# Kernel optimization log

Hardware: AMD Instinct MI355X
Metric: run time of the kernel (lower is better)

## Reference

```python
import jax, jax.numpy as jnp
import numpy as np

EMBED_DIM = 1024
NUM_HEADS = 16
HEAD_DIM = EMBED_DIM // NUM_HEADS
LN_EPS = 1e-12
B, S = 2, 2048


def setup_inputs() -> dict:
    key = jax.random.key(0)
    ks = jax.random.split(key, 12)
    scale = 1.0 / np.sqrt(EMBED_DIM)
    d = EMBED_DIM
    return {
        "in_features": jax.random.normal(ks[0], (B, S, d), dtype=jnp.float32),
        "tgt_mask": jnp.ones((B, S), dtype=jnp.float32),
        "Wq": jax.random.normal(ks[1], (d, d), dtype=jnp.float32) * scale,
        "bq": jnp.zeros((d,), dtype=jnp.float32),
        "Wk": jax.random.normal(ks[2], (d, d), dtype=jnp.float32) * scale,
        "bk": jnp.zeros((d,), dtype=jnp.float32),
        "Wv": jax.random.normal(ks[3], (d, d), dtype=jnp.float32) * scale,
        "bv": jnp.zeros((d,), dtype=jnp.float32),
        "Wo": jax.random.normal(ks[4], (d, d), dtype=jnp.float32) * scale,
        "bo": jnp.zeros((d,), dtype=jnp.float32),
        "gamma": jnp.ones((d,), dtype=jnp.float32),
        "beta": jnp.zeros((d,), dtype=jnp.float32),
    }


def _split_heads(x):  # [B,S,D] -> [B,H,S,Dh]
    b, s, _ = x.shape
    return x.reshape(b, s, NUM_HEADS, HEAD_DIM).transpose(0, 2, 1, 3)


def reference(in_features, tgt_mask, Wq, bq, Wk, bk, Wv, bv, Wo, bo, gamma, beta):
    # Self-attention (tgt_features defaults to in_features). Dropout in eval mode (identity).
    q = _split_heads(in_features @ Wq.T + bq)
    k = _split_heads(in_features @ Wk.T + bk)
    v = _split_heads(in_features @ Wv.T + bv)
    # scores: [B,H,S,S]
    scores = jnp.einsum("bhqd,bhkd->bhqk", q, k) / jnp.sqrt(jnp.float32(HEAD_DIM))
    scores = scores + (1.0 - tgt_mask)[:, None, None, :] * (-100000.0)
    attn = jax.nn.softmax(scores, axis=-1)
    ctx = jnp.einsum("bhqk,bhkd->bhqd", attn, v)  # [B,H,S,Dh]
    ctx = ctx.transpose(0, 2, 1, 3).reshape(in_features.shape)  # merge heads
    out = ctx @ Wo.T + bo
    x = out + in_features
    mu = jnp.mean(x, axis=-1, keepdims=True)
    var = jnp.mean(jnp.square(x - mu), axis=-1, keepdims=True)
    return (x - mu) / jnp.sqrt(var + LN_EPS) * gamma + beta
```

## Files before the change

### kernel.cpp

```cpp
#include <hip/hip_runtime.h>
#include <hip/hip_bf16.h>

#define DM   1024
#define HEADS 16
#define DH    64
#define SEQ  2048
#define BATCH   2
#define LOG2E 1.44269504088896f

typedef __attribute__((ext_vector_type(8))) short short8;
typedef __attribute__((ext_vector_type(4))) short bf16x4;
typedef __attribute__((ext_vector_type(4))) float floatx4;
typedef __attribute__((ext_vector_type(16))) float floatx16;

__device__ __forceinline__ short f2b(float f) {
    union { float f; unsigned u; } v; v.f = f;
    unsigned r = v.u + 0x7FFFu + ((v.u >> 16) & 1u);
    return (short)(r >> 16);
}

#if __has_builtin(__builtin_amdgcn_exp2f)
__device__ __forceinline__ float fexp2(float x) { return __builtin_amdgcn_exp2f(x); }
#else
__device__ __forceinline__ float fexp2(float x) { return exp2f(x); }
#endif

__device__ __forceinline__ void async_copy16(const short* gsrc, short* ldst) {
    __builtin_amdgcn_global_load_lds(
        (const __attribute__((address_space(1))) void*)gsrc,
        (__attribute__((address_space(3))) void*)ldst,
        16, 0, 0);
}

__global__ __launch_bounds__(256) void cvt_all(const float* __restrict__ x,
        const float* __restrict__ wq, const float* __restrict__ wk,
        const float* __restrict__ wv, const float* __restrict__ wo,
        const float* __restrict__ mask,
        short* __restrict__ xb, short* __restrict__ wqkv, short* __restrict__ wob,
        float* __restrict__ maddg)
{
    const int b = blockIdx.x;
    if (b >= 8192) {
        const int bb = b - 8192;
        const float* mrow = mask + (size_t)bb * SEQ;
        float* mg = maddg + (size_t)bb * SEQ;
#pragma unroll
        for (int i = 0; i < 8; ++i) {
            const int idx = threadIdx.x * 8 + i;
            mg[idx] = (1.f - mrow[idx]) * (-100000.f * LOG2E);
        }
        return;
    }
    const float* src; short* dst; int idx;
    if (b < 4096)      { src = x;  dst = xb;                idx = b; }
    else if (b < 5120) { src = wq; dst = wqkv;              idx = b - 4096; }
    else if (b < 6144) { src = wk; dst = wqkv + (1 << 20);  idx = b - 5120; }
    else if (b < 7168) { src = wv; dst = wqkv + (2 << 20);  idx = b - 6144; }
    else               { src = wo; dst = wob;               idx = b - 7168; }
    const int i = idx * 256 + threadIdx.x;
    floatx4 v = ((const floatx4*)src)[i];
    bf16x4 o;
    o.x = f2b(v.x); o.y = f2b(v.y); o.z = f2b(v.z); o.w = f2b(v.w);
    ((bf16x4*)dst)[i] = o;
}

__global__ __launch_bounds__(256) void gemm_qkv(const short* __restrict__ A,
        const short* __restrict__ B,
        const float* __restrict__ bq, const float* __restrict__ bk,
        const float* __restrict__ bv,
        short* __restrict__ qw, short* __restrict__ kw, short* __restrict__ vw)
{
    __shared__ short As[128 * 32];
    __shared__ short Bs[128 * 32];
    const int m0 = blockIdx.x * 128, n0 = blockIdx.y * 128;
    const int w = threadIdx.x >> 6, lane = threadIdx.x & 63;
    const int l16 = lane & 15, quad = lane >> 4;
    const int wm = w >> 1, wn = w & 1;
    const int lr = lane >> 2, lc = (lane & 3) * 8;

    floatx4 acc[4][4];
#pragma unroll
    for (int i = 0; i < 4; ++i)
#pragma unroll
        for (int j = 0; j < 4; ++j) acc[i][j] = (floatx4){0.f, 0.f, 0.f, 0.f};

    for (int kt = 0; kt < DM / 32; ++kt) {
        const int k0 = kt * 32;
        __syncthreads();
        async_copy16(A + (size_t)(m0 + w * 32 + lr) * DM + k0 + lc,      &As[w * 1024]);
        async_copy16(A + (size_t)(m0 + w * 32 + 16 + lr) * DM + k0 + lc, &As[w * 1024 + 512]);
        async_copy16(B + (size_t)(n0 + w * 32 + lr) * DM + k0 + lc,      &Bs[w * 1024]);
        async_copy16(B + (size_t)(n0 + w * 32 + 16 + lr) * DM + k0 + lc, &Bs[w * 1024 + 512]);
        __syncthreads();

        short8 af[4], bf[4];
#pragma unroll
        for (int i = 0; i < 4; ++i)
            af[i] = *(const short8*)&As[(wm * 64 + i * 16 + l16) * 32 + quad * 8];
#pragma unroll
        for (int j = 0; j < 4; ++j)
            bf[j] = *(const short8*)&Bs[(wn * 64 + j * 16 + l16) * 32 + quad * 8];
#pragma unroll
        for (int i = 0; i < 4; ++i)
#pragma unroll
            for (int j = 0; j < 4; ++j)
                acc[i][j] = __builtin_amdgcn_mfma_f32_16x16x32_bf16(af[i], bf[j], acc[i][j], 0, 0, 0);
    }

    const int m_base = m0 + wm * 64 + quad * 4;
#pragma unroll
    for (int j = 0; j < 4; ++j) {
        const int nb = n0 + wn * 64 + j * 16;
        const int t = nb >> 10;
        const int nn = (nb & 1023) + l16;
        const int h = nn >> 6, dh = nn & 63;
        const float* bias = (t == 0) ? bq : (t == 1) ? bk : bv;
        short* dst = (t == 0) ? qw : (t == 1) ? kw : vw;
        const float mulf = (t == 0) ? (0.125f * LOG2E) : 1.0f;
        const float bvv = bias[nn];
#pragma unroll
        for (int i = 0; i < 4; ++i)
#pragma unroll
            for (int r = 0; r < 4; ++r) {
                const int m = m_base + i * 16 + r;
                const int b = m >> 11, s = m & (SEQ - 1);
                dst[(((size_t)(b * HEADS + h)) * SEQ + s) * DH + dh] =
                    f2b((acc[i][j][r] + bvv) * mulf);
            }
    }
}

__global__ __launch_bounds__(256) void transpose_v(const short* __restrict__ v,
                                                   short* __restrict__ vt)
{
    __shared__ short tl[64][72];
    const int st = blockIdx.x;
    const int bh = blockIdx.y;
    const int t = threadIdx.x;
    const int row = t >> 2, off = (t & 3) * 16;
    const short* vp = v + ((size_t)bh * SEQ + st * 64 + row) * DH + off;
    *(short8*)&tl[row][off]     = *(const short8*)vp;
    *(short8*)&tl[row][off + 8] = *(const short8*)(vp + 8);
    __syncthreads();
    short8 o0, o1;
#pragma unroll
    for (int j = 0; j < 8; ++j) { o0[j] = tl[off + j][row]; o1[j] = tl[off + 8 + j][row]; }
    short* op = vt + ((size_t)bh * DH + row) * SEQ + st * 64 + off;
    *(short8*)op = o0;
    *(short8*)(op + 8) = o1;
}

__global__ __launch_bounds__(256) void attn_kernel(const short* __restrict__ q,
        const short* __restrict__ k, const short* __restrict__ vt,
        const float* __restrict__ maddg, short* __restrict__ ctx)
{
    const int id    = blockIdx.x;
    const int qtile = id >> 5;
    const int bh    = id & 31;
    const int bidx  = bh >> 4;
    const int wave = threadIdx.x >> 6, lane = threadIdx.x & 63;
    const int l32 = lane & 31, half = lane >> 5;
    const int kw = wave & 1, qw = wave >> 1;

    __shared__ __align__(16) short smem[20480];
    short* p_lds = smem + 16384;
    short* Ct    = smem;
    float* l_fin = (float*)(smem + 4608);

    const short* kbase0 = k  + (size_t)bh * SEQ * DH;
    const short* vbase0 = vt + (size_t)bh * DH * SEQ;
    const float* mrow   = maddg + (size_t)bidx * SEQ;

    const int qrow = qtile * 64 + qw * 32 + l32;
    const short* qbase = q + ((size_t)bh * SEQ + qrow) * DH;
    short8 b_q[4];
#pragma unroll
    for (int kk = 0; kk < 4; ++kk)
        b_q[kk] = *(const short8*)(qbase + kk * 16 + half * 8);

    floatx16 oacc;
#pragma unroll
    for (int r = 0; r < 16; ++r) oacc[r] = 0.f;
    float l_run = 0.f;

    int srw[2], gg[2];
#pragma unroll
    for (int i = 0; i < 2; ++i) {
        const int slot = i * 256 + wave * 64 + lane;
        srw[i] = slot >> 3;
        gg[i]  = (slot & 7) ^ (srw[i] & 7);
    }

    const int prow = qw * 32 + l32;

    auto stage_kv = [&](int buf, int kt) {
        const short* kbase = kbase0 + (size_t)(kt * 64) * DH;
        const short* vbase = vbase0 + kt * 64;
        const int ko = buf << 12;
        const int vo = 8192 + (buf << 12);
#pragma unroll
        for (int i = 0; i < 2; ++i) {
            async_copy16(kbase + srw[i] * DH + gg[i] * 8,
                         &smem[ko + (i * 256 + wave * 64) * 8]);
            async_copy16(vbase + (size_t)srw[i] * SEQ + gg[i] * 8,
                         &smem[vo + (i * 256 + wave * 64) * 8]);
        }
    };

    stage_kv(0, 0);

    int cur = 0;
    for (int kt = 0; kt < SEQ / 64; ++kt) {
        asm volatile("" ::: "memory");
        __builtin_amdgcn_s_barrier();

        floatx4 md[4];
#pragma unroll
        for (int g = 0; g < 4; ++g)
            md[g] = *(const floatx4*)&mrow[kt * 64 + kw * 32 + 8 * g + 4 * half];
        __builtin_amdgcn_sched_barrier(0);

        if (kt + 1 < SEQ / 64) {
            stage_kv(cur ^ 1, kt + 1);
            asm volatile("s_waitcnt vmcnt(4)" ::: "memory");
        } else {
            asm volatile("s_waitcnt vmcnt(0)" ::: "memory");
        }
        __builtin_amdgcn_s_barrier();

        floatx16 s;
#pragma unroll
        for (int g = 0; g < 4; ++g)
#pragma unroll
            for (int r = 0; r < 4; ++r) s[g * 4 + r] = md[g][r];
        {
            const int ko = cur << 12;
            const int krow = kw * 32 + l32;
            const int ksw = krow & 7;
#pragma unroll
            for (int kk = 0; kk < 4; ++kk) {
                const int c = kk * 2 + half;
                short8 a = *(const short8*)&smem[ko + krow * 64 + ((c ^ ksw) * 8)];
                s = __builtin_amdgcn_mfma_f32_32x32x16_bf16(a, b_q[kk], s, 0, 0, 0);
            }
        }

        float lsum = 0.f;
        const int psw = prow & 7;
#pragma unroll
        for (int g = 0; g < 4; ++g) {
            const float p0 = fexp2(fminf(s[g * 4 + 0], 40.f));
            const float p1 = fexp2(fminf(s[g * 4 + 1], 40.f));
            const float p2 = fexp2(fminf(s[g * 4 + 2], 40.f));
            const float p3 = fexp2(fminf(s[g * 4 + 3], 40.f));
            lsum += (p0 + p1) + (p2 + p3);
            union { __hip_bfloat162 h[2]; bf16x4 v; } u;
            u.h[0] = __float22bfloat162_rn(make_float2(p0, p1));
            u.h[1] = __float22bfloat162_rn(make_float2(p2, p3));
            const int c = kw * 4 + g;
            *(bf16x4*)&p_lds[prow * 64 + ((c ^ psw) * 8) + 4 * half] = u.v;
        }
        l_run += lsum;

        asm volatile("s_waitcnt lgkmcnt(0)" ::: "memory");
        __builtin_amdgcn_s_barrier();

        {
            const int vo = 8192 + (cur << 12);
            const int vrow = kw * 32 + l32;
            const int vsw = vrow & 7;
#pragma unroll
            for (int kk = 0; kk < 4; ++kk) {
                const int c = kk * 2 + half;
                short8 av = *(const short8*)&smem[vo + vrow * 64 + ((c ^ vsw) * 8)];
                short8 bp = *(const short8*)&p_lds[prow * 64 + ((c ^ psw) * 8)];
                oacc = __builtin_amdgcn_mfma_f32_32x32x16_bf16(av, bp, oacc, 0, 0, 0);
            }
        }
        cur ^= 1;
    }

    asm volatile("" ::: "memory");
    __builtin_amdgcn_s_barrier();

    const float l_mine = l_run + __shfl_xor(l_run, 32);
    l_fin[kw * 64 + prow] = l_mine;
    asm volatile("s_waitcnt lgkmcnt(0)" ::: "memory");
    __builtin_amdgcn_s_barrier();

    const int h = bh & 15, bb = bh >> 4;
    const float rl = 1.f / (l_fin[prow] + l_fin[64 + prow]);
#pragma unroll
    for (int g = 0; g < 4; ++g) {
        bf16x4 p;
        p.x = f2b(oacc[g * 4 + 0] * rl);
        p.y = f2b(oacc[g * 4 + 1] * rl);
        p.z = f2b(oacc[g * 4 + 2] * rl);
        p.w = f2b(oacc[g * 4 + 3] * rl);
        const int dh = kw * 32 + 8 * g + 4 * half;
        *(bf16x4*)&Ct[prow * 72 + dh] = p;
    }
    __syncthreads();
    {
        const int row = threadIdx.x >> 2, ch = threadIdx.x & 3;
        short8 v0 = *(const short8*)&Ct[row * 72 + ch * 16];
        short8 v1 = *(const short8*)&Ct[row * 72 + ch * 16 + 8];
        short* gp = ctx + ((size_t)(bb * SEQ + qtile * 64 + row)) * DM + h * 64 + ch * 16;
        *(short8*)gp = v0;
        *(short8*)(gp + 8) = v1;
    }
}

__global__ __launch_bounds__(256) void gemm_o(const short* __restrict__ A,
        const short* __restrict__ B, const float* __restrict__ bo,
        const float* __restrict__ xin, float* __restrict__ out)
{
    __shared__ short As[128 * 32];
    __shared__ short Bs[64 * 32];
    const int m0 = blockIdx.x * 128, n0 = blockIdx.y * 64;
    const int w = threadIdx.x >> 6, lane = threadIdx.x & 63;
    const int l16 = lane & 15, quad = lane >> 4;
    const int wm = w >> 1, wn = w & 1;

    floatx4 acc[4][2];
#pragma unroll
    for (int i = 0; i < 4; ++i)
#pragma unroll
        for (int j = 0; j < 2; ++j) acc[i][j] = (floatx4){0.f, 0.f, 0.f, 0.f};

    const int c0 = w * 64 + lane;

    for (int kt = 0; kt < DM / 32; ++kt) {
        const int k0 = kt * 32;
        __syncthreads();
        {
            const int ra0 = c0 >> 2,          ca0 = (c0 & 3) * 8;
            const int ra1 = (256 + c0) >> 2,  ca1 = (c0 & 3) * 8;
            async_copy16(A + (size_t)(m0 + ra0) * DM + k0 + ca0, &As[(w * 64) * 8]);
            async_copy16(A + (size_t)(m0 + ra1) * DM + k0 + ca1, &As[(256 + w * 64) * 8]);
            const int rb = c0 >> 2, cb = (c0 & 3) * 8;
            async_copy16(B + (size_t)(n0 + rb) * DM + k0 + cb,   &Bs[(w * 64) * 8]);
        }
        __syncthreads();

        short8 af[4], bf[2];
#pragma unroll
        for (int i = 0; i < 4; ++i)
            af[i] = *(const short8*)&As[(wm * 64 + i * 16 + l16) * 32 + quad * 8];
#pragma unroll
        for (int j = 0; j < 2; ++j)
            bf[j] = *(const short8*)&Bs[(wn * 32 + j * 16 + l16) * 32 + quad * 8];
#pragma unroll
        for (int i = 0; i < 4; ++i)
#pragma unroll
            for (int j = 0; j < 2; ++j)
                acc[i][j] = __builtin_amdgcn_mfma_f32_16x16x32_bf16(af[i], bf[j], acc[i][j], 0, 0, 0);
    }

    const int m_base = m0 + wm * 64 + quad * 4;
#pragma unroll
    for (int j = 0; j < 2; ++j) {
        const int n = n0 + wn * 32 + j * 16 + l16;
        const float bvv = bo[n];
#pragma unroll
        for (int i = 0; i < 4; ++i)
#pragma unroll
            for (int r = 0; r < 4; ++r) {
                const int m = m_base + i * 16 + r;
                const size_t idx = (size_t)m * DM + n;
                out[idx] = acc[i][j][r] + bvv + xin[idx];
            }
    }
}

__global__ __launch_bounds__(256) void ln_kernel(float* __restrict__ y,
        const float* __restrict__ gamma, const float* __restrict__ beta)
{
    const int row = blockIdx.x;
    const int t = threadIdx.x;
    const int wave = t >> 6, lane = t & 63;
    const floatx4 v = ((const floatx4*)(y + (size_t)row * DM))[t];
    float s  = v.x + v.y + v.z + v.w;
    float q2 = v.x * v.x + v.y * v.y + v.z * v.z + v.w * v.w;
#pragma unroll
    for (int off = 1; off < 64; off <<= 1) {
        s  += __shfl_xor(s, off);
        q2 += __shfl_xor(q2, off);
    }
    __shared__ float rs[4], rq[4];
    if (lane == 0) { rs[wave] = s; rq[wave] = q2; }
    __syncthreads();
    const float S  = rs[0] + rs[1] + rs[2] + rs[3];
    const float Q2 = rq[0] + rq[1] + rq[2] + rq[3];
    const float mu = S * (1.f / DM);
    float var = Q2 * (1.f / DM) - mu * mu;
    var = fmaxf(var, 0.f);
    const float rstd = rsqrtf(var + 1e-12f);
    const floatx4 g = ((const floatx4*)gamma)[t];
    const floatx4 bt = ((const floatx4*)beta)[t];
    floatx4 o;
    o.x = (v.x - mu) * rstd * g.x + bt.x;
    o.y = (v.y - mu) * rstd * g.y + bt.y;
    o.z = (v.z - mu) * rstd * g.z + bt.z;
    o.w = (v.w - mu) * rstd * g.w + bt.w;
    ((floatx4*)(y + (size_t)row * DM))[t] = o;
}

extern "C" void kernel_launch(void* const* d_in, const int* in_sizes, int n_in,
                              void* d_out, int out_size, void* d_ws, size_t ws_size,
                              hipStream_t stream) {
    const float* x     = (const float*)d_in[0];
    const float* mask  = (const float*)d_in[1];
    const float* Wq    = (const float*)d_in[2];
    const float* bq    = (const float*)d_in[3];
    const float* Wk    = (const float*)d_in[4];
    const float* bk    = (const float*)d_in[5];
    const float* Wv    = (const float*)d_in[6];
    const float* bv    = (const float*)d_in[7];
    const float* Wo    = (const float*)d_in[8];
    const float* bo    = (const float*)d_in[9];
    const float* gamma = (const float*)d_in[10];
    const float* beta  = (const float*)d_in[11];
    float* out = (float*)d_out;

    const size_t NTOK = (size_t)BATCH * SEQ * DM;
    const size_t WSZ  = (size_t)DM * DM;
    short* xb   = (short*)d_ws;
    short* wqkv = xb + NTOK;
    short* wob  = wqkv + 3 * WSZ;
    short* qw   = wob + WSZ;
    short* kw   = qw + NTOK;
    short* vw   = kw + NTOK;
    short* vtw  = vw + NTOK;
    short* ctxw = vw;
    float* maddg = (float*)(vtw + NTOK);

    dim3 blk(256);
    cvt_all<<<dim3(8194), blk, 0, stream>>>(x, Wq, Wk, Wv, Wo, mask, xb, wqkv, wob, maddg);
    gemm_qkv<<<dim3(32, 24), blk, 0, stream>>>(xb, wqkv, bq, bk, bv, qw, kw, vw);
    transpose_v<<<dim3(SEQ / 64, BATCH * HEADS), blk, 0, stream>>>(vw, vtw);
    attn_kernel<<<dim3(32 * 32), blk, 0, stream>>>(qw, kw, vtw, maddg, ctxw);
    gemm_o<<<dim3(32, 16), blk, 0, stream>>>(ctxw, wob, bo, x, out);
    ln_kernel<<<BATCH * SEQ, blk, 0, stream>>>(out, gamma, beta);
}
```

Measured before the change: 226.1 us.

## Keep attention probabilities in registers via permlane32 swap, two waves per block

```diff
diff --git a/kernel.cpp b/kernel.cpp
--- a/kernel.cpp
+++ b/kernel.cpp
@@ -30,6 +30,16 @@
         (const __attribute__((address_space(1))) void*)gsrc,
         (__attribute__((address_space(3))) void*)ldst,
         16, 0, 0);
+}
+
+__device__ __forceinline__ unsigned pk2(float lo, float hi) {
+    union { __hip_bfloat162 h; unsigned u; } x;
+    x.h = __float22bfloat162_rn(make_float2(lo, hi));
+    return x.u;
+}
+
+__device__ __forceinline__ void pl32swap(unsigned& a, unsigned& b) {
+    asm volatile("v_permlane32_swap_b32 %0, %1" : "+v"(a), "+v"(b));
 }
 
 __global__ __launch_bounds__(256) void cvt_all(const float* __restrict__ x,
@@ -150,7 +160,7 @@
     *(short8*)(op + 8) = o1;
 }
 
-__global__ __launch_bounds__(256) void attn_kernel(const short* __restrict__ q,
+__global__ __launch_bounds__(128) void attn_kernel(const short* __restrict__ q,
         const short* __restrict__ k, const short* __restrict__ vt,
         const float* __restrict__ maddg, short* __restrict__ ctx)
 {
@@ -160,38 +170,38 @@
     const int bidx  = bh >> 4;
     const int wave = threadIdx.x >> 6, lane = threadIdx.x & 63;
     const int l32 = lane & 31, half = lane >> 5;
-    const int kw = wave & 1, qw = wave >> 1;
-
-    __shared__ __align__(16) short smem[20480];
-    short* p_lds = smem + 16384;
-    short* Ct    = smem;
-    float* l_fin = (float*)(smem + 4608);
+
+    __shared__ __align__(16) short smem[16384];
+    short* Ct = smem;
 
     const short* kbase0 = k  + (size_t)bh * SEQ * DH;
     const short* vbase0 = vt + (size_t)bh * DH * SEQ;
     const float* mrow   = maddg + (size_t)bidx * SEQ;
 
-    const int qrow = qtile * 64 + qw * 32 + l32;
+    const int qrow = qtile * 64 + wave * 32 + l32;
     const short* qbase = q + ((size_t)bh * SEQ + qrow) * DH;
     short8 b_q[4];
 #pragma unroll
     for (int kk = 0; kk < 4; ++kk)
         b_q[kk] = *(const short8*)(qbase + kk * 16 + half * 8);
 
-    floatx16 oacc;
-#pragma unroll
-    for (int r = 0; r < 16; ++r) oacc[r] = 0.f;
+    floatx16 oacc[2];
+#pragma unroll
+    for (int db = 0; db < 2; ++db)
+#pragma unroll
+        for (int r = 0; r < 16; ++r) oacc[db][r] = 0.f;
     float l_run = 0.f;
 
-    int srw[2], gg[2];
-#pragma unroll
-    for (int i = 0; i < 2; ++i) {
-        const int slot = i * 256 + wave * 64 + lane;
+    int srw[4], gg[4];
+#pragma unroll
+    for (int i = 0; i < 4; ++i) {
+        const int slot = i * 128 + threadIdx.x;
         srw[i] = slot >> 3;
         gg[i]  = (slot & 7) ^ (srw[i] & 7);
     }
 
-    const int prow = qw * 32 + l32;
+    const int prow = wave * 32 + l32;
+    const int lsw  = l32 & 7;
 
     auto stage_kv = [&](int buf, int kt) {
         const short* kbase = kbase0 + (size_t)(kt * 64) * DH;
@@ -199,11 +209,11 @@
         const int ko = buf << 12;
         const int vo = 8192 + (buf << 12);
 #pragma unroll
-        for (int i = 0; i < 2; ++i) {
+        for (int i = 0; i < 4; ++i) {
             async_copy16(kbase + srw[i] * DH + gg[i] * 8,
-                         &smem[ko + (i * 256 + wave * 64) * 8]);
+                         &smem[ko + (i * 128 + wave * 64) * 8]);
             async_copy16(vbase + (size_t)srw[i] * SEQ + gg[i] * 8,
-                         &smem[vo + (i * 256 + wave * 64) * 8]);
+                         &smem[vo + (i * 128 + wave * 64) * 8]);
         }
     };
 
@@ -214,67 +224,84 @@
         asm volatile("" ::: "memory");
         __builtin_amdgcn_s_barrier();
 
-        floatx4 md[4];
-#pragma unroll
-        for (int g = 0; g < 4; ++g)
-            md[g] = *(const floatx4*)&mrow[kt * 64 + kw * 32 + 8 * g + 4 * half];
+        floatx4 md[2][4];
+#pragma unroll
+        for (int kb = 0; kb < 2; ++kb)
+#pragma unroll
+            for (int g = 0; g < 4; ++g)
+                md[kb][g] = *(const floatx4*)&mrow[kt * 64 + kb * 32 + 8 * g + 4 * half];
         __builtin_amdgcn_sched_barrier(0);
 
         if (kt + 1 < SEQ / 64) {
             stage_kv(cur ^ 1, kt + 1);
-            asm volatile("s_waitcnt vmcnt(4)" ::: "memory");
+            asm volatile("s_waitcnt vmcnt(8)" ::: "memory");
         } else {
             asm volatile("s_waitcnt vmcnt(0)" ::: "memory");
         }
         __builtin_amdgcn_s_barrier();
 
-        floatx16 s;
-#pragma unroll
-        for (int g = 0; g < 4; ++g)
-#pragma unroll
-            for (int r = 0; r < 4; ++r) s[g * 4 + r] = md[g][r];
+        floatx16 sf[2];
+#pragma unroll
+        for (int kb = 0; kb < 2; ++kb)
+#pragma unroll
+            for (int g = 0; g < 4; ++g)
+#pragma unroll
+                for (int r = 0; r < 4; ++r) sf[kb][g * 4 + r] = md[kb][g][r];
         {
             const int ko = cur << 12;
-            const int krow = kw * 32 + l32;
-            const int ksw = krow & 7;
-#pragma unroll
-            for (int kk = 0; kk < 4; ++kk) {
-                const int c = kk * 2 + half;
-                short8 a = *(const short8*)&smem[ko + krow * 64 + ((c ^ ksw) * 8)];
-                s = __builtin_amdgcn_mfma_f32_32x32x16_bf16(a, b_q[kk], s, 0, 0, 0);
-            }
-        }
-
+#pragma unroll
+            for (int kb = 0; kb < 2; ++kb) {
+                const int krow = kb * 32 + l32;
+#pragma unroll
+                for (int kk = 0; kk < 4; ++kk) {
+                    const int c = kk * 2 + half;
+                    short8 a = *(const short8*)&smem[ko + krow * 64 + ((c ^ lsw) * 8)];
+                    sf[kb] = __builtin_amdgcn_mfma_f32_32x32x16_bf16(a, b_q[kk], sf[kb], 0, 0, 0);
+                }
+            }
+        }
+
+        unsigned w0[2][4], w1[2][4];
         float lsum = 0.f;
-        const int psw = prow & 7;
-#pragma unroll
-        for (int g = 0; g < 4; ++g) {
-            const float p0 = fexp2(fminf(s[g * 4 + 0], 40.f));
-            const float p1 = fexp2(fminf(s[g * 4 + 1], 40.f));
-            const float p2 = fexp2(fminf(s[g * 4 + 2], 40.f));
-            const float p3 = fexp2(fminf(s[g * 4 + 3], 40.f));
-            lsum += (p0 + p1) + (p2 + p3);
-            union { __hip_bfloat162 h[2]; bf16x4 v; } u;
-            u.h[0] = __float22bfloat162_rn(make_float2(p0, p1));
-            u.h[1] = __float22bfloat162_rn(make_float2(p2, p3));
-            const int c = kw * 4 + g;
-            *(bf16x4*)&p_lds[prow * 64 + ((c ^ psw) * 8) + 4 * half] = u.v;
-        }
+#pragma unroll
+        for (int kb = 0; kb < 2; ++kb)
+#pragma unroll
+            for (int g = 0; g < 4; ++g) {
+                const float p0 = fexp2(fminf(sf[kb][g * 4 + 0], 40.f));
+                const float p1 = fexp2(fminf(sf[kb][g * 4 + 1], 40.f));
+                const float p2 = fexp2(fminf(sf[kb][g * 4 + 2], 40.f));
+                const float p3 = fexp2(fminf(sf[kb][g * 4 + 3], 40.f));
+                lsum += (p0 + p1) + (p2 + p3);
+                w0[kb][g] = pk2(p0, p1);
+                w1[kb][g] = pk2(p2, p3);
+            }
         l_run += lsum;
 
-        asm volatile("s_waitcnt lgkmcnt(0)" ::: "memory");
-        __builtin_amdgcn_s_barrier();
+#pragma unroll
+        for (int kb = 0; kb < 2; ++kb)
+#pragma unroll
+            for (int kp = 0; kp < 2; ++kp) {
+                pl32swap(w0[kb][2 * kp], w0[kb][2 * kp + 1]);
+                pl32swap(w1[kb][2 * kp], w1[kb][2 * kp + 1]);
+            }
 
         {
             const int vo = 8192 + (cur << 12);
-            const int vrow = kw * 32 + l32;
-            const int vsw = vrow & 7;
-#pragma unroll
-            for (int kk = 0; kk < 4; ++kk) {
-                const int c = kk * 2 + half;
-                short8 av = *(const short8*)&smem[vo + vrow * 64 + ((c ^ vsw) * 8)];
-                short8 bp = *(const short8*)&p_lds[prow * 64 + ((c ^ psw) * 8)];
-                oacc = __builtin_amdgcn_mfma_f32_32x32x16_bf16(av, bp, oacc, 0, 0, 0);
+#pragma unroll
+            for (int db = 0; db < 2; ++db) {
+                const int vrow = db * 32 + l32;
+#pragma unroll
+                for (int kk = 0; kk < 4; ++kk) {
+                    const int c = kk * 2 + half;
+                    short8 av = *(const short8*)&smem[vo + vrow * 64 + ((c ^ lsw) * 8)];
+                    const int kb = kk >> 1, kp = kk & 1;
+                    union { unsigned u[4]; short8 v; } bu;
+                    bu.u[0] = w0[kb][2 * kp];
+                    bu.u[1] = w1[kb][2 * kp];
+                    bu.u[2] = w0[kb][2 * kp + 1];
+                    bu.u[3] = w1[kb][2 * kp + 1];
+                    oacc[db] = __builtin_amdgcn_mfma_f32_32x32x16_bf16(av, bu.v, oacc[db], 0, 0, 0);
+                }
             }
         }
         cur ^= 1;
@@ -283,31 +310,28 @@
     asm volatile("" ::: "memory");
     __builtin_amdgcn_s_barrier();
 
-    const float l_mine = l_run + __shfl_xor(l_run, 32);
-    l_fin[kw * 64 + prow] = l_mine;
-    asm volatile("s_waitcnt lgkmcnt(0)" ::: "memory");
-    __builtin_amdgcn_s_barrier();
+    const float rl = 1.f / (l_run + __shfl_xor(l_run, 32));
 
     const int h = bh & 15, bb = bh >> 4;
-    const float rl = 1.f / (l_fin[prow] + l_fin[64 + prow]);
-#pragma unroll
-    for (int g = 0; g < 4; ++g) {
-        bf16x4 p;
-        p.x = f2b(oacc[g * 4 + 0] * rl);
-        p.y = f2b(oacc[g * 4 + 1] * rl);
-        p.z = f2b(oacc[g * 4 + 2] * rl);
-        p.w = f2b(oacc[g * 4 + 3] * rl);
-        const int dh = kw * 32 + 8 * g + 4 * half;
-        *(bf16x4*)&Ct[prow * 72 + dh] = p;
-    }
+#pragma unroll
+    for (int db = 0; db < 2; ++db)
+#pragma unroll
+        for (int g = 0; g < 4; ++g) {
+            bf16x4 p;
+            p.x = f2b(oacc[db][g * 4 + 0] * rl);
+            p.y = f2b(oacc[db][g * 4 + 1] * rl);
+            p.z = f2b(oacc[db][g * 4 + 2] * rl);
+            p.w = f2b(oacc[db][g * 4 + 3] * rl);
+            const int dh = db * 32 + 8 * g + 4 * half;
+            *(bf16x4*)&Ct[prow * 72 + dh] = p;
+        }
     __syncthreads();
     {
-        const int row = threadIdx.x >> 2, ch = threadIdx.x & 3;
-        short8 v0 = *(const short8*)&Ct[row * 72 + ch * 16];
-        short8 v1 = *(const short8*)&Ct[row * 72 + ch * 16 + 8];
-        short* gp = ctx + ((size_t)(bb * SEQ + qtile * 64 + row)) * DM + h * 64 + ch * 16;
-        *(short8*)gp = v0;
-        *(short8*)(gp + 8) = v1;
+        const int row = threadIdx.x >> 1, off = (threadIdx.x & 1) * 32;
+        short* gp = ctx + ((size_t)(bb * SEQ + qtile * 64 + row)) * DM + h * 64 + off;
+#pragma unroll
+        for (int j = 0; j < 4; ++j)
+            *(short8*)(gp + 8 * j) = *(const short8*)&Ct[row * 72 + off + 8 * j];
     }
 }
 
@@ -439,7 +463,7 @@
     cvt_all<<<dim3(8194), blk, 0, stream>>>(x, Wq, Wk, Wv, Wo, mask, xb, wqkv, wob, maddg);
     gemm_qkv<<<dim3(32, 24), blk, 0, stream>>>(xb, wqkv, bq, bk, bv, qw, kw, vw);
     transpose_v<<<dim3(SEQ / 64, BATCH * HEADS), blk, 0, stream>>>(vw, vtw);
-    attn_kernel<<<dim3(32 * 32), blk, 0, stream>>>(qw, kw, vtw, maddg, ctxw);
+    attn_kernel<<<dim3(32 * 32), dim3(128), 0, stream>>>(qw, kw, vtw, maddg, ctxw);
     gemm_o<<<dim3(32, 16), blk, 0, stream>>>(ctxw, wob, bo, x, out);
     ln_kernel<<<BATCH * SEQ, blk, 0, stream>>>(out, gamma, beta);
 }
```

After: 237.9 us. 1.05x slower.

## Single-buffer V with in-iteration load, preload mask into LDS

Applied to the files above, without the earlier changes.

```diff
diff --git a/kernel.cpp b/kernel.cpp
--- a/kernel.cpp
+++ b/kernel.cpp
@@ -163,9 +163,10 @@
     const int kw = wave & 1, qw = wave >> 1;
 
     __shared__ __align__(16) short smem[20480];
-    short* p_lds = smem + 16384;
-    short* Ct    = smem;
-    float* l_fin = (float*)(smem + 4608);
+    short* p_lds    = smem + 12288;
+    float* mask_lds = (float*)(smem + 16384);
+    short* Ct       = smem;
+    float* l_fin    = (float*)(smem + 4608);
 
     const short* kbase0 = k  + (size_t)bh * SEQ * DH;
     const short* vbase0 = vt + (size_t)bh * DH * SEQ;
@@ -193,21 +194,27 @@
 
     const int prow = qw * 32 + l32;
 
-    auto stage_kv = [&](int buf, int kt) {
+    auto stage_k = [&](int buf, int kt) {
         const short* kbase = kbase0 + (size_t)(kt * 64) * DH;
-        const short* vbase = vbase0 + kt * 64;
         const int ko = buf << 12;
-        const int vo = 8192 + (buf << 12);
-#pragma unroll
-        for (int i = 0; i < 2; ++i) {
+#pragma unroll
+        for (int i = 0; i < 2; ++i)
             async_copy16(kbase + srw[i] * DH + gg[i] * 8,
                          &smem[ko + (i * 256 + wave * 64) * 8]);
+    };
+    auto stage_v = [&](int kt) {
+        const short* vbase = vbase0 + kt * 64;
+#pragma unroll
+        for (int i = 0; i < 2; ++i)
             async_copy16(vbase + (size_t)srw[i] * SEQ + gg[i] * 8,
-                         &smem[vo + (i * 256 + wave * 64) * 8]);
-        }
+                         &smem[8192 + (i * 256 + wave * 64) * 8]);
     };
 
-    stage_kv(0, 0);
+#pragma unroll
+    for (int i = 0; i < 2; ++i)
+        async_copy16((const short*)mrow + (i * 256 + threadIdx.x) * 8,
+                     &smem[16384 + (i * 256 + wave * 64) * 8]);
+    stage_k(0, 0);
 
     int cur = 0;
     for (int kt = 0; kt < SEQ / 64; ++kt) {
@@ -217,14 +224,16 @@
         floatx4 md[4];
 #pragma unroll
         for (int g = 0; g < 4; ++g)
-            md[g] = *(const floatx4*)&mrow[kt * 64 + kw * 32 + 8 * g + 4 * half];
+            md[g] = *(const floatx4*)&mask_lds[kt * 64 + kw * 32 + 8 * g + 4 * half];
+
+        stage_v(kt);
         __builtin_amdgcn_sched_barrier(0);
-
-        if (kt + 1 < SEQ / 64) {
-            stage_kv(cur ^ 1, kt + 1);
+        const bool has_next = (kt + 1 < SEQ / 64);
+        if (has_next) {
+            stage_k(cur ^ 1, kt + 1);
             asm volatile("s_waitcnt vmcnt(4)" ::: "memory");
         } else {
-            asm volatile("s_waitcnt vmcnt(0)" ::: "memory");
+            asm volatile("s_waitcnt vmcnt(2)" ::: "memory");
         }
         __builtin_amdgcn_s_barrier();
 
@@ -263,16 +272,20 @@
         l_run += lsum;
 
         asm volatile("s_waitcnt lgkmcnt(0)" ::: "memory");
+        if (has_next) {
+            asm volatile("s_waitcnt vmcnt(2)" ::: "memory");
+        } else {
+            asm volatile("s_waitcnt vmcnt(0)" ::: "memory");
+        }
         __builtin_amdgcn_s_barrier();
 
         {
-            const int vo = 8192 + (cur << 12);
             const int vrow = kw * 32 + l32;
             const int vsw = vrow & 7;
 #pragma unroll
             for (int kk = 0; kk < 4; ++kk) {
                 const int c = kk * 2 + half;
-                short8 av = *(const short8*)&smem[vo + vrow * 64 + ((c ^ vsw) * 8)];
+                short8 av = *(const short8*)&smem[8192 + vrow * 64 + ((c ^ vsw) * 8)];
                 short8 bp = *(const short8*)&p_lds[prow * 64 + ((c ^ psw) * 8)];
                 oacc = __builtin_amdgcn_mfma_f32_32x32x16_bf16(av, bp, oacc, 0, 0, 0);
             }
```

Result: faster. 217.1 us, median of 7 (-4.0%).
